# Kernel tuning notes

Measured on AMD Instinct MI355X. Metric: run time of the kernel, lower is better.

Reference implementation:

```python
import jax, jax.numpy as jnp
import numpy as np

EMBED = 256; HEADS = 8; LEVELS = 4; POINTS = 4; DIM = EMBED // HEADS


def _bilinear_gather(vflat, H, W, px, py):
    """grid_sample(mode='bilinear', padding='zeros', align_corners=False).
    vflat: (bs, heads, H*W, d); px, py: (bs, heads, nq, P) pixel coords.
    Returns (bs, heads, nq, P, d).
    """
    x0 = jnp.floor(px); y0 = jnp.floor(py)
    x1 = x0 + 1.0;      y1 = y0 + 1.0
    wx1 = px - x0; wx0 = 1.0 - wx1
    wy1 = py - y0; wy0 = 1.0 - wy1

    def corner(ix, iy, w):
        valid = (ix >= 0) & (ix <= W - 1) & (iy >= 0) & (iy <= H - 1)
        idx = (jnp.clip(iy, 0, H - 1) * W + jnp.clip(ix, 0, W - 1)).astype(jnp.int32)
        b, h, nq, P = idx.shape
        g = jnp.take_along_axis(vflat, idx.reshape(b, h, nq * P)[..., None], axis=2)
        g = g.reshape(b, h, nq, P, -1)
        return g * (w * valid)[..., None]

    return (corner(x0, y0, wx0 * wy0) + corner(x1, y0, wx1 * wy0)
            + corner(x0, y1, wx0 * wy1) + corner(x1, y1, wx1 * wy1))


def _ms_deform_attn(value4, shapes, loc, attn):
    """value4 (bs,nv,heads,D); loc (bs,nq,heads,L,P,2) in [0,1];
    attn (bs,nq,heads,L,P). Returns (bs,nq,heads*D)."""
    bs, nq = loc.shape[0], loc.shape[1]
    grids = 2.0 * loc - 1.0
    attn_t = jnp.transpose(attn, (0, 2, 1, 3, 4))  # (bs,heads,nq,L,P)
    out = jnp.zeros((bs, HEADS, nq, DIM), value4.dtype)
    start = 0
    for lvl in range(LEVELS):
        H, W = int(shapes[lvl, 0]), int(shapes[lvl, 1])
        v = value4[:, start:start + H * W]                 # (bs,HW,heads,D)
        vflat = jnp.transpose(v, (0, 2, 1, 3))             # (bs,heads,HW,D)
        g = jnp.transpose(grids[:, :, :, lvl], (0, 2, 1, 3, 4))  # (bs,heads,nq,P,2)
        px = (g[..., 0] + 1.0) * (W * 0.5) - 0.5
        py = (g[..., 1] + 1.0) * (H * 0.5) - 0.5
        sampled = _bilinear_gather(vflat, H, W, px, py)    # (bs,heads,nq,P,D)
        out = out + jnp.einsum('bhqpd,bhqp->bhqd', sampled, attn_t[:, :, :, lvl])
        start += H * W
    return jnp.transpose(out, (0, 2, 1, 3)).reshape(bs, nq, HEADS * DIM)


def _forward(query, value, query_pos, reference_points, last_reference_offsets,
             shapes, Wv, bv, Wo, bo, Wa, ba, Wout, bout):
    identity = query
    q = query + query_pos
    bs, nq, _ = q.shape
    nv = value.shape[1]
    v = (value @ Wv + bv).reshape(bs, nv, HEADS, DIM)
    off = (q @ Wo + bo).reshape(bs, nq, HEADS, LEVELS, POINTS, 2)
    attn = jax.nn.softmax((q @ Wa + ba).reshape(bs, nq, HEADS, LEVELS * POINTS), axis=-1)
    attn = attn.reshape(bs, nq, HEADS, LEVELS, POINTS)
    wh = jnp.asarray(np.asarray(shapes)[:, ::-1].copy(), jnp.float32)  # (L,2) as (w,h)
    loc = (reference_points[:, :, None, :, None, :]
           + off / wh[None, None, None, :, None, :]
           + last_reference_offsets[:, :, :, None, None, :])  # flow-guided per-head shift
    out = _ms_deform_attn(v, shapes, loc, attn)
    return out @ Wout + bout + identity  # dropout is identity at eval


def setup_inputs() -> dict:
    key = jax.random.key(0)
    ks = jax.random.split(key, 10)
    bs, nq = 8, 1200
    shapes = np.array([[92, 160], [46, 80], [23, 40], [12, 20]], np.int64)
    nv = int((shapes[:, 0] * shapes[:, 1]).sum())
    f = jnp.float32
    return {
        "query": jax.random.normal(ks[0], (bs, nq, EMBED), f),
        "value": jax.random.normal(ks[1], (bs, nv, EMBED), f),
        "query_pos": jax.random.normal(ks[2], (bs, nq, EMBED), f),
        "reference_points": jax.random.uniform(ks[3], (bs, nq, LEVELS, 2), f),
        "last_reference_offsets": jax.random.normal(ks[4], (bs, nq, HEADS, 2), f) * 0.02,
        "spatial_shapes": shapes,
        "Wv": jax.random.normal(ks[5], (EMBED, EMBED), f) * 0.02,
        "bv": jnp.zeros((EMBED,), f),
        "Wo": jax.random.normal(ks[6], (EMBED, HEADS * LEVELS * POINTS * 2), f) * 0.02,
        "bo": jax.random.normal(ks[7], (HEADS * LEVELS * POINTS * 2,), f) * 0.02,
        "Wa": jax.random.normal(ks[8], (EMBED, HEADS * LEVELS * POINTS), f) * 0.02,
        "ba": jnp.zeros((HEADS * LEVELS * POINTS,), f),
        "Wout": jax.random.normal(ks[9], (EMBED, EMBED), f) * 0.02,
        "bout": jnp.zeros((EMBED,), f),
    }


def reference(query, value, query_pos, reference_points, last_reference_offsets,
              spatial_shapes, Wv, bv, Wo, bo, Wa, ba, Wout, bout):
    return _forward(query, value, query_pos, reference_points, last_reference_offsets,
                    spatial_shapes, Wv, bv, Wo, bo, Wa, ba, Wout, bout)
```

## Files before the change

kernel.cpp:

```cpp
#include <hip/hip_runtime.h>
#include <math.h>

#define BS 8
#define NQ 1200
#define NV 19560
#define EMB 256
#define TPB 153

typedef __bf16 bf16;
typedef bf16 bf16x8 __attribute__((ext_vector_type(8)));
typedef float f32x4 __attribute__((ext_vector_type(4)));
typedef float f32x16 __attribute__((ext_vector_type(16)));

static __device__ __forceinline__ bf16x8 cvt8(float4 a, float4 b) {
    bf16x8 r;
    r[0] = (bf16)a.x; r[1] = (bf16)a.y; r[2] = (bf16)a.z; r[3] = (bf16)a.w;
    r[4] = (bf16)b.x; r[5] = (bf16)b.y; r[6] = (bf16)b.z; r[7] = (bf16)b.w;
    return r;
}

static __device__ __forceinline__ void gl16(const void* g, void* l) {
    __builtin_amdgcn_global_load_lds(
        (const __attribute__((address_space(1))) void*)g,
        (__attribute__((address_space(3))) void*)l, 16, 0, 0);
}

__global__ __launch_bounds__(256) void prep_k(
    const float* __restrict__ Wv, const float* __restrict__ Wo,
    const float* __restrict__ Wa, const float* __restrict__ Wout,
    const float* __restrict__ query, const float* __restrict__ qpos,
    const float* __restrict__ bo, const float* __restrict__ ba,
    bf16* __restrict__ Wv_p, bf16* __restrict__ Wo_p,
    bf16* __restrict__ Wa_p, bf16* __restrict__ Wout_p,
    bf16* __restrict__ qsum, float* __restrict__ cb)
{
    int bid = blockIdx.x, tid = threadIdx.x;
    if (bid < 896) {
        const float* src; bf16* dst; int N, t0;
        if (bid < 256)      { src = Wv;   dst = Wv_p;   N = 256; t0 = bid * 256; }
        else if (bid < 512) { src = Wo;   dst = Wo_p;   N = 256; t0 = (bid - 256) * 256; }
        else if (bid < 640) { src = Wa;   dst = Wa_p;   N = 128; t0 = (bid - 512) * 256; }
        else                { src = Wout; dst = Wout_p; N = 256; t0 = (bid - 640) * 256; }
        int t = t0 + tid;
        int n = t >> 8, k = t & 255;
        dst[t] = (bf16)src[k * N + n];
    } else if (bid < 10496) {
        int t = (bid - 896) * 256 + tid;
        qsum[t] = (bf16)(query[t] + qpos[t]);
    } else {
        cb[tid] = bo[tid];
        if (tid < 128) cb[256 + tid] = ba[tid];
    }
}

__global__ __launch_bounds__(256, 1) void vgemm_k(
    const float* __restrict__ A, const bf16* __restrict__ Bp,
    const float* __restrict__ bias, bf16* __restrict__ outB, int Mtiles)
{
    __shared__ __align__(16) bf16  sB[256 * 256];
    __shared__ __align__(16) float sA[4 * 2 * 1024];
    const int tid = threadIdx.x;
    const int lane = tid & 63;
    const int w = tid >> 6;
    const int l16 = lane & 15;
    const int qd = lane >> 4;

#pragma unroll
    for (int i = 0; i < 32; ++i) {
        int s = i * 256 + tid;
        int r = s >> 5, p = s & 31, c = p ^ (r & 7);
        gl16(Bp + (size_t)r * 256 + c * 8, sB + ((size_t)i * 256 + w * 64) * 8);
    }

    float* sAw = sA + w * 2048;
    const int arow = lane >> 3;
    const int aslot = (lane & 7) ^ arow;
    auto stageT = [&](int t_, int kg, int buf) {
        int b_ = t_ / TPB, p0_ = (t_ - b_ * TPB) * 128;
#pragma unroll
        for (int i = 0; i < 4; ++i) {
            int pix = min(p0_ + w * 32 + i * 8 + arow, NV - 1);
            gl16(A + ((size_t)b_ * NV + pix) * 256 + kg * 32 + aslot * 4,
                 sAw + buf * 1024 + i * 256);
        }
    };

    int t = blockIdx.x;
    stageT(t, 0, 0);
    stageT(t, 1, 1);

    float bb[16];
#pragma unroll
    for (int ct = 0; ct < 16; ++ct) bb[ct] = bias[ct * 16 + l16];

    __syncthreads();

    const int akey = l16 & 7;
    f32x4 acc0[16], acc1[16];

    auto compute = [&](int kg, int buf) {
        const float* ab = sAw + buf * 1024;
        const float* ar0 = ab + l16 * 32;
        const float* ar1 = ab + (16 + l16) * 32;
        float4 a00 = *(const float4*)(ar0 + ((qd * 2    ) ^ akey) * 4);
        float4 a01 = *(const float4*)(ar0 + ((qd * 2 + 1) ^ akey) * 4);
        float4 a10 = *(const float4*)(ar1 + ((qd * 2    ) ^ akey) * 4);
        float4 a11 = *(const float4*)(ar1 + ((qd * 2 + 1) ^ akey) * 4);
        bf16x8 af0 = cvt8(a00, a01);
        bf16x8 af1 = cvt8(a10, a11);
#pragma unroll
        for (int ct = 0; ct < 16; ++ct) {
            int brow = ct * 16 + l16;
            bf16x8 bfr = *(const bf16x8*)(sB + (size_t)brow * 256 +
                                          ((kg * 4 + qd) ^ (brow & 7)) * 8);
            acc0[ct] = __builtin_amdgcn_mfma_f32_16x16x32_bf16(af0, bfr, acc0[ct], 0, 0, 0);
            acc1[ct] = __builtin_amdgcn_mfma_f32_16x16x32_bf16(af1, bfr, acc1[ct], 0, 0, 0);
        }
    };

#define VM_WAIT4 asm volatile("s_waitcnt vmcnt(4)" ::: "memory")

    while (true) {
#pragma unroll
        for (int ct = 0; ct < 16; ++ct) {
            acc0[ct] = (f32x4){0.f, 0.f, 0.f, 0.f};
            acc1[ct] = (f32x4){0.f, 0.f, 0.f, 0.f};
        }

        int tn = t + gridDim.x;
        const bool last = (tn >= Mtiles);

        VM_WAIT4; compute(0, 0); stageT(t, 2, 0);
        VM_WAIT4; compute(1, 1); stageT(t, 3, 1);
        VM_WAIT4; compute(2, 0); stageT(t, 4, 0);
        VM_WAIT4; compute(3, 1); stageT(t, 5, 1);
        VM_WAIT4; compute(4, 0); stageT(t, 6, 0);
        VM_WAIT4; compute(5, 1); stageT(t, 7, 1);
        VM_WAIT4; compute(6, 0); if (!last) stageT(tn, 0, 0);
        VM_WAIT4; compute(7, 1); if (!last) stageT(tn, 1, 1);

        int b = t / TPB, p0 = (t - b * TPB) * 128;
#pragma unroll
        for (int ct = 0; ct < 16; ++ct) {
            const bf16* dst0 = outB + ((size_t)(b * 8 + (ct >> 1)) * NV) * 32 + (ct & 1) * 16 + l16;
#pragma unroll
            for (int r = 0; r < 4; ++r) {
                int pix0 = p0 + w * 32 + qd * 4 + r;
                if (pix0 < NV)
                    *(bf16*)(dst0 + (size_t)pix0 * 32) = (bf16)(acc0[ct][r] + bb[ct]);
                int pix1 = pix0 + 16;
                if (pix1 < NV)
                    *(bf16*)(dst0 + (size_t)pix1 * 32) = (bf16)(acc1[ct][r] + bb[ct]);
            }
        }

        if (last) break;
        t = tn;
    }
#undef VM_WAIT4
}

template <int NS, int NB, int NGRP, bool HAS_RES, bool OUT_BF16>
__global__ __launch_bounds__(256, 2) void gemm3_k(
    const bf16* __restrict__ Ah, const bf16* __restrict__ Bp,
    const float* __restrict__ bias, const float* __restrict__ res,
    float* __restrict__ outF, bf16* __restrict__ outB, int Mtiles)
{
    constexpr int CT = NB / 16;
    __shared__ __align__(16) bf16 sB[NB * 256];
    const int tid = threadIdx.x;
    const int lane = tid & 63;
    const int w = tid >> 6;
    const int l16 = lane & 15;
    const int qd = lane >> 4;
    const int col0 = (blockIdx.x % NGRP) * NB;
    const int tstride = gridDim.x / NGRP;
    const bf16* Bsrc = Bp + (size_t)col0 * 256;

    uint4 curH[8], nxtH[8];
    auto loadA = [&](int t, uint4* dH) {
        size_t rb = ((size_t)t * 64 + w * 16 + l16) * 256;
#pragma unroll
        for (int kc = 0; kc < 8; ++kc)
            dH[kc] = *(const uint4*)(Ah + rb + kc * 32 + qd * 8);
    };

    int tile = blockIdx.x / NGRP;
    if (tile < Mtiles) loadA(tile, curH);

#pragma unroll
    for (int i = 0; i < NB * 32 / 256; ++i) {
        int s = i * 256 + tid;
        int r = s >> 5, p = s & 31, c = p ^ (r & 7);
        gl16(Bsrc + (size_t)r * 256 + c * 8, sB + (size_t)(i * 256 + w * 64) * 8);
    }
    __syncthreads();

    for (; tile < Mtiles; tile += tstride) {
        int nt = tile + tstride;
        if (nt < Mtiles) loadA(nt, nxtH);

        f32x4 acc[CT];
#pragma unroll
        for (int c = 0; c < CT; ++c) acc[c] = (f32x4){0.f, 0.f, 0.f, 0.f};
#pragma unroll
        for (int kc = 0; kc < 8; ++kc) {
            bf16x8 af = *(const bf16x8*)&curH[kc];
#pragma unroll
            for (int ct = 0; ct < CT; ++ct) {
                int brow = ct * 16 + l16;
                int chunk = (kc * 4 + qd) ^ (l16 & 7);
                bf16x8 bfr = *(const bf16x8*)(sB + (size_t)brow * 256 + chunk * 8);
                acc[ct] = __builtin_amdgcn_mfma_f32_16x16x32_bf16(af, bfr, acc[ct], 0, 0, 0);
            }
        }
#pragma unroll
        for (int ct = 0; ct < CT; ++ct) {
            int col = col0 + ct * 16 + l16;
            float bbv = bias[col];
#pragma unroll
            for (int r = 0; r < 4; ++r) {
                int row = tile * 64 + w * 16 + qd * 4 + r;
                size_t idx = (size_t)row * NS + col;
                float v = acc[ct][r] + bbv;
                if (HAS_RES) v += res[(size_t)row * 256 + col];
                if (OUT_BF16) outB[idx] = (bf16)v;
                else          outF[idx] = v;
            }
        }
#pragma unroll
        for (int i = 0; i < 8; ++i) curH[i] = nxtH[i];
    }
}

static __device__ __forceinline__ void b8f(uint4 u, float* f) {
    f[0] = __uint_as_float(u.x << 16); f[1] = __uint_as_float(u.x & 0xffff0000u);
    f[2] = __uint_as_float(u.y << 16); f[3] = __uint_as_float(u.y & 0xffff0000u);
    f[4] = __uint_as_float(u.z << 16); f[5] = __uint_as_float(u.z & 0xffff0000u);
    f[6] = __uint_as_float(u.w << 16); f[7] = __uint_as_float(u.w & 0xffff0000u);
}

__global__ __launch_bounds__(256) void sample4_k(
    const bf16* __restrict__ vv, const float* __restrict__ comb,
    const float* __restrict__ refp, const float* __restrict__ lref,
    bf16* __restrict__ outb)
{
    const int cH[4] = {92, 46, 23, 12};
    const int cW[4] = {160, 80, 40, 20};
    const int cS[4] = {0, 14720, 18400, 19320};
    const int w = threadIdx.x >> 6;
    const int lane = threadIdx.x & 63;
    const int wid = blockIdx.x * 4 + w;
    const int bq = wid >> 3, h = wid & 7;
    const int b = bq / NQ;
    const int p = lane >> 2, dg = lane & 3;
    const int lvl = p >> 2;

    float logit = comb[(size_t)bq * 384 + 256 + h * 16 + p];
    float mx = logit;
#pragma unroll
    for (int s = 4; s < 64; s <<= 1) mx = fmaxf(mx, __shfl_xor(mx, s));
    float e = __expf(logit - mx);
    float ssum = e;
#pragma unroll
    for (int s = 4; s < 64; s <<= 1) ssum += __shfl_xor(ssum, s);
    float wgt = e / ssum;

    const int Hh = cH[lvl], Ww = cW[lvl];
    float ox = comb[(size_t)bq * 384 + h * 32 + p * 2];
    float oy = comb[(size_t)bq * 384 + h * 32 + p * 2 + 1];
    float rx = refp[(size_t)bq * 8 + lvl * 2];
    float ry = refp[(size_t)bq * 8 + lvl * 2 + 1];
    float lrx = lref[(size_t)bq * 16 + h * 2];
    float lry = lref[(size_t)bq * 16 + h * 2 + 1];

    float px = (rx + ox / (float)Ww + lrx) * (float)Ww - 0.5f;
    float py = (ry + oy / (float)Hh + lry) * (float)Hh - 0.5f;
    float x0f = floorf(px), y0f = floorf(py);
    int x0 = (int)x0f, y0 = (int)y0f;
    float wx1 = px - x0f, wx0 = 1.f - wx1;
    float wy1 = py - y0f, wy0 = 1.f - wy1;
    bool xa = (unsigned)x0 < (unsigned)Ww, xb = (unsigned)(x0 + 1) < (unsigned)Ww;
    bool ya = (unsigned)y0 < (unsigned)Hh, yb = (unsigned)(y0 + 1) < (unsigned)Hh;
    int xc0 = min(max(x0, 0), Ww - 1), xc1 = min(max(x0 + 1, 0), Ww - 1);
    int yc0 = min(max(y0, 0), Hh - 1), yc1 = min(max(y0 + 1, 0), Hh - 1);
    float w00 = wgt * wx0 * wy0 * (float)(xa && ya);
    float w01 = wgt * wx1 * wy0 * (float)(xb && ya);
    float w10 = wgt * wx0 * wy1 * (float)(xa && yb);
    float w11 = wgt * wx1 * wy1 * (float)(xb && yb);

    const bf16* vb = vv + ((size_t)(b * 8 + h) * NV + cS[lvl]) * 32 + dg * 8;
    uint4 g00 = *(const uint4*)(vb + ((size_t)yc0 * Ww + xc0) * 32);
    uint4 g01 = *(const uint4*)(vb + ((size_t)yc0 * Ww + xc1) * 32);
    uint4 g10 = *(const uint4*)(vb + ((size_t)yc1 * Ww + xc0) * 32);
    uint4 g11 = *(const uint4*)(vb + ((size_t)yc1 * Ww + xc1) * 32);

    float acc[8], f[8];
    b8f(g00, f);
#pragma unroll
    for (int j = 0; j < 8; j++) acc[j] = w00 * f[j];
    b8f(g01, f);
#pragma unroll
    for (int j = 0; j < 8; j++) acc[j] = fmaf(w01, f[j], acc[j]);
    b8f(g10, f);
#pragma unroll
    for (int j = 0; j < 8; j++) acc[j] = fmaf(w10, f[j], acc[j]);
    b8f(g11, f);
#pragma unroll
    for (int j = 0; j < 8; j++) acc[j] = fmaf(w11, f[j], acc[j]);

#pragma unroll
    for (int s = 4; s < 64; s <<= 1)
#pragma unroll
        for (int j = 0; j < 8; j++) acc[j] += __shfl_xor(acc[j], s);

    if (p == 0) {
        bf16x8 o;
#pragma unroll
        for (int j = 0; j < 8; j++) o[j] = (bf16)acc[j];
        *(bf16x8*)(outb + (size_t)bq * 256 + h * 32 + dg * 8) = o;
    }
}

extern "C" void kernel_launch(void* const* d_in, const int* in_sizes, int n_in,
                              void* d_out, int out_size, void* d_ws, size_t ws_size,
                              hipStream_t stream) {
    (void)in_sizes; (void)n_in; (void)out_size; (void)ws_size;
    const float* query = (const float*)d_in[0];
    const float* value = (const float*)d_in[1];
    const float* qpos  = (const float*)d_in[2];
    const float* refp  = (const float*)d_in[3];
    const float* lref  = (const float*)d_in[4];
    const float* Wv   = (const float*)d_in[6];
    const float* bv   = (const float*)d_in[7];
    const float* Wo   = (const float*)d_in[8];
    const float* bo   = (const float*)d_in[9];
    const float* Wa   = (const float*)d_in[10];
    const float* ba   = (const float*)d_in[11];
    const float* Wout = (const float*)d_in[12];
    const float* bout = (const float*)d_in[13];

    char* ws = (char*)d_ws;
    bf16*  Wv_p   = (bf16*)(ws + 0);
    bf16*  Wo_p   = (bf16*)(ws + 131072);
    bf16*  Wa_p   = (bf16*)(ws + 262144);
    bf16*  Wout_p = (bf16*)(ws + 327680);
    bf16*  qsum   = (bf16*)(ws + 458752);
    float* comb   = (float*)(ws + 5373952);
    bf16*  tsa_b  = (bf16*)(ws + 20119552);
    bf16*  v_b    = (bf16*)(ws + 25034752);
    float* cbias  = (float*)(ws + 105152512);

    prep_k<<<10497, 256, 0, stream>>>(Wv, Wo, Wa, Wout, query, qpos, bo, ba,
                                      Wv_p, Wo_p, Wa_p, Wout_p, qsum, cbias);

    vgemm_k<<<256, 256, 0, stream>>>(value, Wv_p, bv, v_b, BS * TPB);
    gemm3_k<384, 128, 3, false, false><<<450, 256, 0, stream>>>(
        qsum, Wo_p, cbias, nullptr, comb, nullptr, (BS * NQ) / 64);
    sample4_k<<<(BS * NQ * 8) / 4, 256, 0, stream>>>(v_b, comb, refp, lref, tsa_b);
    gemm3_k<256, 128, 2, true, false><<<300, 256, 0, stream>>>(
        tsa_b, Wout_p, bout, query, (float*)d_out, nullptr, (BS * NQ) / 64);
}
```

Before: 396.5 us.

## Vectorize value-projection stores and pair adjacent pixels in the deformable sampler

The value-projection GEMM swaps its MFMA operands so each lane holds four consecutive output channels. It then writes bf16x4 vectors instead of scattered 2-byte stores, starts the accumulators from the bias, and uses a padded per-head row count so the tail tile needs no bounds checks. The sampler gives each point 8 lanes covering two horizontally adjacent pixels, so each bilinear corner pair comes from one contiguous 128-byte span. This halves the gather loads per point, and the first two pipeline stages relax their vmcnt waits. The cost is a slightly larger workspace, an x-clamp to W-2 that relies on per-lane weight selection at the borders, and more per-lane index arithmetic in the sampler.

```diff
diff --git a/kernel.cpp b/kernel.cpp
--- a/kernel.cpp
+++ b/kernel.cpp
@@ -4,13 +4,14 @@
 #define BS 8
 #define NQ 1200
 #define NV 19560
+#define NVP 19584
 #define EMB 256
 #define TPB 153
 
 typedef __bf16 bf16;
 typedef bf16 bf16x8 __attribute__((ext_vector_type(8)));
+typedef bf16 bf16x4 __attribute__((ext_vector_type(4)));
 typedef float f32x4 __attribute__((ext_vector_type(4)));
-typedef float f32x16 __attribute__((ext_vector_type(16)));
 
 static __device__ __forceinline__ bf16x8 cvt8(float4 a, float4 b) {
     bf16x8 r;
@@ -89,9 +90,10 @@
     stageT(t, 0, 0);
     stageT(t, 1, 1);
 
-    float bb[16];
-#pragma unroll
-    for (int ct = 0; ct < 16; ++ct) bb[ct] = bias[ct * 16 + l16];
+    f32x4 bias4[16];
+#pragma unroll
+    for (int ct = 0; ct < 16; ++ct)
+        bias4[ct] = *(const f32x4*)(bias + ct * 16 + qd * 4);
 
     __syncthreads();
 
@@ -113,50 +115,47 @@
             int brow = ct * 16 + l16;
             bf16x8 bfr = *(const bf16x8*)(sB + (size_t)brow * 256 +
                                           ((kg * 4 + qd) ^ (brow & 7)) * 8);
-            acc0[ct] = __builtin_amdgcn_mfma_f32_16x16x32_bf16(af0, bfr, acc0[ct], 0, 0, 0);
-            acc1[ct] = __builtin_amdgcn_mfma_f32_16x16x32_bf16(af1, bfr, acc1[ct], 0, 0, 0);
+            acc0[ct] = __builtin_amdgcn_mfma_f32_16x16x32_bf16(bfr, af0, acc0[ct], 0, 0, 0);
+            acc1[ct] = __builtin_amdgcn_mfma_f32_16x16x32_bf16(bfr, af1, acc1[ct], 0, 0, 0);
         }
     };
 
-#define VM_WAIT4 asm volatile("s_waitcnt vmcnt(4)" ::: "memory")
+#define VM_WAIT36 asm volatile("s_waitcnt vmcnt(36)" ::: "memory")
+#define VM_WAIT4  asm volatile("s_waitcnt vmcnt(4)"  ::: "memory")
 
     while (true) {
 #pragma unroll
-        for (int ct = 0; ct < 16; ++ct) {
-            acc0[ct] = (f32x4){0.f, 0.f, 0.f, 0.f};
-            acc1[ct] = (f32x4){0.f, 0.f, 0.f, 0.f};
-        }
+        for (int ct = 0; ct < 16; ++ct) { acc0[ct] = bias4[ct]; acc1[ct] = bias4[ct]; }
 
         int tn = t + gridDim.x;
         const bool last = (tn >= Mtiles);
 
-        VM_WAIT4; compute(0, 0); stageT(t, 2, 0);
-        VM_WAIT4; compute(1, 1); stageT(t, 3, 1);
-        VM_WAIT4; compute(2, 0); stageT(t, 4, 0);
-        VM_WAIT4; compute(3, 1); stageT(t, 5, 1);
-        VM_WAIT4; compute(4, 0); stageT(t, 6, 0);
-        VM_WAIT4; compute(5, 1); stageT(t, 7, 1);
-        VM_WAIT4; compute(6, 0); if (!last) stageT(tn, 0, 0);
-        VM_WAIT4; compute(7, 1); if (!last) stageT(tn, 1, 1);
+        VM_WAIT36; compute(0, 0); stageT(t, 2, 0);
+        VM_WAIT36; compute(1, 1); stageT(t, 3, 1);
+        VM_WAIT4;  compute(2, 0); stageT(t, 4, 0);
+        VM_WAIT4;  compute(3, 1); stageT(t, 5, 1);
+        VM_WAIT4;  compute(4, 0); stageT(t, 6, 0);
+        VM_WAIT4;  compute(5, 1); stageT(t, 7, 1);
+        VM_WAIT4;  compute(6, 0); if (!last) stageT(tn, 0, 0);
+        VM_WAIT4;  compute(7, 1); if (!last) stageT(tn, 1, 1);
 
         int b = t / TPB, p0 = (t - b * TPB) * 128;
+        int pix0 = p0 + w * 32 + l16;
 #pragma unroll
         for (int ct = 0; ct < 16; ++ct) {
-            const bf16* dst0 = outB + ((size_t)(b * 8 + (ct >> 1)) * NV) * 32 + (ct & 1) * 16 + l16;
-#pragma unroll
-            for (int r = 0; r < 4; ++r) {
-                int pix0 = p0 + w * 32 + qd * 4 + r;
-                if (pix0 < NV)
-                    *(bf16*)(dst0 + (size_t)pix0 * 32) = (bf16)(acc0[ct][r] + bb[ct]);
-                int pix1 = pix0 + 16;
-                if (pix1 < NV)
-                    *(bf16*)(dst0 + (size_t)pix1 * 32) = (bf16)(acc1[ct][r] + bb[ct]);
-            }
+            bf16* dst = outB + ((size_t)(b * 8 + (ct >> 1)) * NVP) * 32
+                             + (ct & 1) * 16 + qd * 4;
+            bf16x4 v0, v1;
+#pragma unroll
+            for (int r = 0; r < 4; ++r) { v0[r] = (bf16)acc0[ct][r]; v1[r] = (bf16)acc1[ct][r]; }
+            *(bf16x4*)(dst + (size_t)pix0 * 32)        = v0;
+            *(bf16x4*)(dst + (size_t)(pix0 + 16) * 32) = v1;
         }
 
         if (last) break;
         t = tn;
     }
+#undef VM_WAIT36
 #undef VM_WAIT4
 }
 
@@ -253,72 +252,77 @@
     const int wid = blockIdx.x * 4 + w;
     const int bq = wid >> 3, h = wid & 7;
     const int b = bq / NQ;
-    const int p = lane >> 2, dg = lane & 3;
-    const int lvl = p >> 2;
-
-    float logit = comb[(size_t)bq * 384 + 256 + h * 16 + p];
-    float mx = logit;
-#pragma unroll
-    for (int s = 4; s < 64; s <<= 1) mx = fmaxf(mx, __shfl_xor(mx, s));
-    float e = __expf(logit - mx);
-    float ssum = e;
-#pragma unroll
-    for (int s = 4; s < 64; s <<= 1) ssum += __shfl_xor(ssum, s);
-    float wgt = e / ssum;
-
-    const int Hh = cH[lvl], Ww = cW[lvl];
-    float ox = comb[(size_t)bq * 384 + h * 32 + p * 2];
-    float oy = comb[(size_t)bq * 384 + h * 32 + p * 2 + 1];
-    float rx = refp[(size_t)bq * 8 + lvl * 2];
-    float ry = refp[(size_t)bq * 8 + lvl * 2 + 1];
+    const int ps = lane >> 3;
+    const int dg8 = lane & 7;
+    const int hx2 = dg8 >> 2;
+
+    float lg0 = comb[(size_t)bq * 384 + 256 + h * 16 + ps];
+    float lg1 = comb[(size_t)bq * 384 + 256 + h * 16 + 8 + ps];
+    float mx = fmaxf(lg0, lg1);
+#pragma unroll
+    for (int s = 8; s < 64; s <<= 1) mx = fmaxf(mx, __shfl_xor(mx, s));
+    float e0 = __expf(lg0 - mx), e1 = __expf(lg1 - mx);
+    float ss = e0 + e1;
+#pragma unroll
+    for (int s = 8; s < 64; s <<= 1) ss += __shfl_xor(ss, s);
+    float inv = 1.f / ss;
+
+    float acc[8];
+#pragma unroll
+    for (int j = 0; j < 8; j++) acc[j] = 0.f;
+
+    const float* rp = refp + (size_t)bq * 8;
     float lrx = lref[(size_t)bq * 16 + h * 2];
     float lry = lref[(size_t)bq * 16 + h * 2 + 1];
 
-    float px = (rx + ox / (float)Ww + lrx) * (float)Ww - 0.5f;
-    float py = (ry + oy / (float)Hh + lry) * (float)Hh - 0.5f;
-    float x0f = floorf(px), y0f = floorf(py);
-    int x0 = (int)x0f, y0 = (int)y0f;
-    float wx1 = px - x0f, wx0 = 1.f - wx1;
-    float wy1 = py - y0f, wy0 = 1.f - wy1;
-    bool xa = (unsigned)x0 < (unsigned)Ww, xb = (unsigned)(x0 + 1) < (unsigned)Ww;
-    bool ya = (unsigned)y0 < (unsigned)Hh, yb = (unsigned)(y0 + 1) < (unsigned)Hh;
-    int xc0 = min(max(x0, 0), Ww - 1), xc1 = min(max(x0 + 1, 0), Ww - 1);
-    int yc0 = min(max(y0, 0), Hh - 1), yc1 = min(max(y0 + 1, 0), Hh - 1);
-    float w00 = wgt * wx0 * wy0 * (float)(xa && ya);
-    float w01 = wgt * wx1 * wy0 * (float)(xb && ya);
-    float w10 = wgt * wx0 * wy1 * (float)(xa && yb);
-    float w11 = wgt * wx1 * wy1 * (float)(xb && yb);
-
-    const bf16* vb = vv + ((size_t)(b * 8 + h) * NV + cS[lvl]) * 32 + dg * 8;
-    uint4 g00 = *(const uint4*)(vb + ((size_t)yc0 * Ww + xc0) * 32);
-    uint4 g01 = *(const uint4*)(vb + ((size_t)yc0 * Ww + xc1) * 32);
-    uint4 g10 = *(const uint4*)(vb + ((size_t)yc1 * Ww + xc0) * 32);
-    uint4 g11 = *(const uint4*)(vb + ((size_t)yc1 * Ww + xc1) * 32);
-
-    float acc[8], f[8];
-    b8f(g00, f);
-#pragma unroll
-    for (int j = 0; j < 8; j++) acc[j] = w00 * f[j];
-    b8f(g01, f);
-#pragma unroll
-    for (int j = 0; j < 8; j++) acc[j] = fmaf(w01, f[j], acc[j]);
-    b8f(g10, f);
-#pragma unroll
-    for (int j = 0; j < 8; j++) acc[j] = fmaf(w10, f[j], acc[j]);
-    b8f(g11, f);
-#pragma unroll
-    for (int j = 0; j < 8; j++) acc[j] = fmaf(w11, f[j], acc[j]);
+#pragma unroll
+    for (int s2 = 0; s2 < 2; ++s2) {
+        int p = s2 * 8 + ps;
+        int lvl = p >> 2;
+        const int Hh = cH[lvl], Ww = cW[lvl];
+        float ox = comb[(size_t)bq * 384 + h * 32 + p * 2];
+        float oy = comb[(size_t)bq * 384 + h * 32 + p * 2 + 1];
+        float rx = rp[lvl * 2], ry = rp[lvl * 2 + 1];
+
+        float px = (rx + ox / (float)Ww + lrx) * (float)Ww - 0.5f;
+        float py = (ry + oy / (float)Hh + lry) * (float)Hh - 0.5f;
+        float x0f = floorf(px), y0f = floorf(py);
+        int x0 = (int)x0f, y0 = (int)y0f;
+        float wx1 = px - x0f, wx0 = 1.f - wx1;
+        float wy1 = py - y0f, wy0 = 1.f - wy1;
+        bool xa = (unsigned)x0 < (unsigned)Ww, xb = (unsigned)(x0 + 1) < (unsigned)Ww;
+        bool ya = (unsigned)y0 < (unsigned)Hh, yb = (unsigned)(y0 + 1) < (unsigned)Hh;
+        int px0 = min(max(x0, 0), Ww - 2);
+        int hx = px0 + hx2;
+        float wxh = (hx == x0 && xa) ? wx0 : ((hx == x0 + 1 && xb) ? wx1 : 0.f);
+        int yc0 = min(max(y0, 0), Hh - 1), yc1 = min(max(y0 + 1, 0), Hh - 1);
+        float wgt = (s2 ? e1 : e0) * inv;
+        float wA = wgt * wy0 * (ya ? 1.f : 0.f) * wxh;
+        float wB = wgt * wy1 * (yb ? 1.f : 0.f) * wxh;
+
+        const bf16* base = vv + ((size_t)(b * 8 + h) * NVP + cS[lvl]) * 32 + dg8 * 8;
+        uint4 gA = *(const uint4*)(base + ((size_t)yc0 * Ww + px0) * 32);
+        uint4 gB = *(const uint4*)(base + ((size_t)yc1 * Ww + px0) * 32);
+
+        float f[8];
+        b8f(gA, f);
+#pragma unroll
+        for (int j = 0; j < 8; j++) acc[j] = fmaf(wA, f[j], acc[j]);
+        b8f(gB, f);
+#pragma unroll
+        for (int j = 0; j < 8; j++) acc[j] = fmaf(wB, f[j], acc[j]);
+    }
 
 #pragma unroll
     for (int s = 4; s < 64; s <<= 1)
 #pragma unroll
         for (int j = 0; j < 8; j++) acc[j] += __shfl_xor(acc[j], s);
 
-    if (p == 0) {
+    if (lane < 4) {
         bf16x8 o;
 #pragma unroll
         for (int j = 0; j < 8; j++) o[j] = (bf16)acc[j];
-        *(bf16x8*)(outb + (size_t)bq * 256 + h * 32 + dg * 8) = o;
+        *(bf16x8*)(outb + (size_t)bq * 256 + h * 32 + lane * 8) = o;
     }
 }
 
@@ -349,7 +353,7 @@
     float* comb   = (float*)(ws + 5373952);
     bf16*  tsa_b  = (bf16*)(ws + 20119552);
     bf16*  v_b    = (bf16*)(ws + 25034752);
-    float* cbias  = (float*)(ws + 105152512);
+    float* cbias  = (float*)(ws + 105250816);
 
     prep_k<<<10497, 256, 0, stream>>>(Wv, Wo, Wa, Wout, query, qpos, bo, ba,
                                       Wv_p, Wo_p, Wa_p, Wout_p, qsum, cbias);
```

New measurement: 393.2 us. Within noise of the previous version (-0.8%).
